# Optimization experiments

Measured on AMD Instinct MI355X. Metric: run time of the kernel, lower is better.

## Reference

```python
import jax, jax.numpy as jnp
import numpy as np

N = 100000   # nodes
E = 1600000  # edges
IN, HID, OUT = 128, 128, 64


def setup_inputs() -> dict:
    key = jax.random.key(0)
    ks = jax.random.split(key, 8)
    x = jax.random.normal(ks[0], (N, IN), dtype=jnp.float32)
    edge_index = jax.random.randint(ks[1], (2, E), 0, N, dtype=jnp.int64)
    W1 = jax.random.normal(ks[2], (IN, HID), dtype=jnp.float32) * 0.05
    b1 = jnp.zeros((HID,), dtype=jnp.float32)
    W2 = jax.random.normal(ks[3], (HID, OUT), dtype=jnp.float32) * 0.05
    b2 = jnp.zeros((OUT,), dtype=jnp.float32)
    Wd = jax.random.normal(ks[4], (OUT, IN), dtype=jnp.float32) * 0.05
    bd = jnp.zeros((IN,), dtype=jnp.float32)
    return {"x": x, "edge_index": edge_index, "W1": W1, "b1": b1,
            "W2": W2, "b2": b2, "Wd": Wd, "bd": bd}


def _gcn_conv(x, src, dst, W, b):
    # PyG GCNConv: add self-loops, symmetric normalization D^-1/2 (A+I) D^-1/2,
    # messages flow src -> dst, aggregated by sum at dst.
    h = x @ W                                   # [N, F]
    ones = jnp.ones((src.shape[0],), x.dtype)
    deg = jax.ops.segment_sum(ones, dst, num_segments=N) + 1.0  # +1 for self-loop
    dinv = jax.lax.rsqrt(deg)                   # deg^-1/2, [N]
    coef = dinv[src] * dinv[dst]                # per-edge norm
    agg = jax.ops.segment_sum(h[src] * coef[:, None], dst, num_segments=N)
    agg = agg + h * (dinv * dinv)[:, None]      # self-loop contribution
    return agg + b


def reference(x, edge_index, W1, b1, W2, b2, Wd, bd):
    src, dst = edge_index[0], edge_index[1]
    h = jax.nn.relu(_gcn_conv(x, src, dst, W1, b1))
    # dropout in eval mode -> identity
    z = _gcn_conv(h, src, dst, W2, b2)          # [N, OUT] embedding
    x_recon = z @ Wd + bd                        # [N, IN]
    return (x_recon, z)
```

## Files before the change

### kernel.cpp

```cpp
#include <hip/hip_runtime.h>
#include <hip/hip_bf16.h>
#include <hip/hip_fp16.h>


#define TPB 256
#define CAP 64

typedef float v2f __attribute__((ext_vector_type(2)));


__device__ __forceinline__ unsigned short f2bf(float f) {
    unsigned u = __float_as_uint(f);
    unsigned r = u + 0x7fffu + ((u >> 16) & 1u);
    return (unsigned short)(r >> 16);
}
__device__ __forceinline__ float bf_lo(unsigned u) { return __uint_as_float(u << 16); }
__device__ __forceinline__ float bf_hi(unsigned u) { return __uint_as_float(u & 0xffff0000u); }


template <int K, int C, int TN, bool BIAS, bool INBF, bool OUTBF>
__device__ __forceinline__ void gemm_body(const void* __restrict__ Ap,
                                          const float* __restrict__ W,
                                          const float* __restrict__ bias,
                                          void* __restrict__ outp, int N, int bid,
                                          float* __restrict__ Ws) {
    constexpr int BM  = 128;
    constexpr int TM  = 8;
    constexpr int BK  = 32;
    constexpr int NCT = C / TN;
    static_assert(NCT * (BM / TM) == TPB, "thread layout");

    int tid = threadIdx.x;
    int tc = tid % NCT;
    int tr = tid / NCT;
    int c0 = tc * TN;
    int r0 = bid * BM + tr * TM;

    float acc[TM][TN] = {};

    for (int k0 = 0; k0 < K; k0 += BK) {
        __syncthreads();
        for (int i = tid * 4; i < BK * C; i += TPB * 4)
            *(float4*)&Ws[i] = *(const float4*)&W[k0 * C + i];
        __syncthreads();

        for (int k = 0; k < BK; k += 4) {
            float4 a[TM];
            uint2  au[TM];
#pragma unroll
            for (int i = 0; i < TM; ++i) {
                int r = r0 + i;
                if (r >= N) r = N - 1;
                if (INBF)
                    au[i] = *(const uint2*)((const unsigned short*)Ap + (size_t)r * K + k0 + k);
                else
                    a[i] = *(const float4*)((const float*)Ap + (size_t)r * K + k0 + k);
            }
#pragma unroll
            for (int kk = 0; kk < 4; ++kk) {
                float w[TN];
#pragma unroll
                for (int j = 0; j < TN; j += 4)
                    *(float4*)&w[j] = *(const float4*)&Ws[(k + kk) * C + c0 + j];
#pragma unroll
                for (int i = 0; i < TM; ++i) {
                    float av;
                    if (INBF) {
                        unsigned uu = (kk < 2) ? au[i].x : au[i].y;
                        av = (kk & 1) ? bf_hi(uu) : bf_lo(uu);
                    } else {
                        av = ((const float*)&a[i])[kk];
                    }
#pragma unroll
                    for (int j = 0; j < TN; ++j) acc[i][j] += av * w[j];
                }
            }
        }
    }

#pragma unroll
    for (int i = 0; i < TM; ++i) {
        int r = r0 + i;
        if (r >= N) continue;
        if (BIAS) {
#pragma unroll
            for (int j = 0; j < TN; ++j) acc[i][j] += bias[c0 + j];
        }
        if (OUTBF) {
            unsigned short* ob = (unsigned short*)outp + (size_t)r * C + c0;
            unsigned pk[TN / 2];
#pragma unroll
            for (int j = 0; j < TN; j += 2)
                pk[j / 2] = (unsigned)f2bf(acc[i][j]) | ((unsigned)f2bf(acc[i][j + 1]) << 16);
            if (TN == 8)      *(uint4*)ob = *(uint4*)pk;
            else if (TN == 4) *(uint2*)ob = *(uint2*)pk;
        } else {
            float* of = (float*)outp + (size_t)r * C + c0;
#pragma unroll
            for (int j = 0; j < TN; j += 4)
                *(float4*)&of[j] = *(float4*)&acc[i][j];
        }
    }
}

template <int K, int C, int TN, bool BIAS, bool INBF, bool OUTBF>
__global__ __launch_bounds__(TPB) void gemm_k(const void* __restrict__ Ap,
                                              const float* __restrict__ W,
                                              const float* __restrict__ bias,
                                              void* __restrict__ outp, int N) {
    __shared__ float Ws[32 * C];
    gemm_body<K, C, TN, BIAS, INBF, OUTBF>(Ap, W, bias, outp, N, blockIdx.x, Ws);
}


__global__ __launch_bounds__(TPB) void fused1_k(const float* __restrict__ x,
                                                const float* __restrict__ W1,
                                                unsigned* __restrict__ h1b,
                                                const int* __restrict__ src,
                                                const int* __restrict__ dst,
                                                int* __restrict__ cnt,
                                                unsigned* __restrict__ bucket,
                                                int N, int E, int gb) {
    __shared__ float Ws[32 * 128];
    if ((int)blockIdx.x < gb) {
        gemm_body<128, 128, 8, false, false, true>(x, W1, nullptr, h1b, N, blockIdx.x, Ws);
    } else {
        int bid = (int)blockIdx.x - gb;
        int e0 = (bid * TPB + (int)threadIdx.x) * 8;
        if (e0 + 7 < E) {
            int4 sa = *(const int4*)&src[e0];
            int4 sb = *(const int4*)&src[e0 + 4];
            int4 da = *(const int4*)&dst[e0];
            int4 db = *(const int4*)&dst[e0 + 4];
            int ss[8] = {sa.x, sa.y, sa.z, sa.w, sb.x, sb.y, sb.z, sb.w};
            int dd[8] = {da.x, da.y, da.z, da.w, db.x, db.y, db.z, db.w};
            int rr[8];
#pragma unroll
            for (int q = 0; q < 8; ++q) rr[q] = atomicAdd(&cnt[dd[q]], 1);
#pragma unroll
            for (int q = 0; q < 8; ++q)
                if (rr[q] < CAP) bucket[(size_t)dd[q] * CAP + rr[q]] = (unsigned)ss[q];
        } else {
            for (int e = e0; e < E; ++e) {
                int s = src[e], d = dst[e];
                int r = atomicAdd(&cnt[d], 1);
                if (r < CAP) bucket[(size_t)d * CAP + r] = (unsigned)s;
            }
        }
    }
}


template <int F2, bool RELU, bool OUTBF>
__global__ __launch_bounds__(TPB) void agg_k(const unsigned* __restrict__ h,
                                             const int* __restrict__ cnt,
                                             const unsigned* __restrict__ bucket,
                                             const float* __restrict__ bias,
                                             void* __restrict__ outp, int N) {
    constexpr int NPB = TPB / F2;
    int ln = threadIdx.x / F2;
    int f2 = threadIdx.x % F2;
    int n  = blockIdx.x * NPB + ln;
    if (n >= N) return;

    int cfull = cnt[n];
    float di = rsqrtf((float)cfull + 1.0f);
    unsigned us = h[(size_t)n * F2 + f2];
    float ax = bf_lo(us) * (di * di);
    float ay = bf_hi(us) * (di * di);

    int cn = cfull < CAP ? cfull : CAP;
    const unsigned* bk = bucket + (size_t)n * CAP;

    int j = 0;
    for (; j + 7 < cn; j += 8) {
        int s[8], cs[8];
        unsigned v[8];
#pragma unroll
        for (int q = 0; q < 8; ++q) s[q] = (int)bk[j + q];
#pragma unroll
        for (int q = 0; q < 8; ++q) {
            v[q]  = h[(size_t)s[q] * F2 + f2];
            cs[q] = cnt[s[q]];
        }
#pragma unroll
        for (int q = 0; q < 8; ++q) {
            float c = rsqrtf((float)cs[q] + 1.0f) * di;
            ax += c * bf_lo(v[q]);
            ay += c * bf_hi(v[q]);
        }
    }
    for (; j < cn; ++j) {
        int s = (int)bk[j];
        unsigned v = h[(size_t)s * F2 + f2];
        float c = rsqrtf((float)cnt[s] + 1.0f) * di;
        ax += c * bf_lo(v);
        ay += c * bf_hi(v);
    }

    float rx = ax + bias[2 * f2];
    float ry = ay + bias[2 * f2 + 1];
    if (RELU) { rx = fmaxf(rx, 0.f); ry = fmaxf(ry, 0.f); }
    if (OUTBF) {
        unsigned pk = (unsigned)f2bf(rx) | ((unsigned)f2bf(ry) << 16);
        ((unsigned*)outp)[(size_t)n * F2 + f2] = pk;
    } else {
        v2f r; r.x = rx; r.y = ry;
        __builtin_nontemporal_store(r, (v2f*)outp + (size_t)n * F2 + f2);
    }
}


extern "C" void kernel_launch(void* const* d_in, const int* in_sizes, int n_in,
                              void* d_out, int out_size, void* d_ws, size_t ws_size,
                              hipStream_t stream) {
    const float* x    = (const float*)d_in[0];
    const int*   eidx = (const int*)d_in[1];
    const float* W1   = (const float*)d_in[2];
    const float* b1   = (const float*)d_in[3];
    const float* W2   = (const float*)d_in[4];
    const float* b2   = (const float*)d_in[5];
    const float* Wd   = (const float*)d_in[6];
    const float* bd   = (const float*)d_in[7];

    const int N = in_sizes[0] / 128;
    const int E = in_sizes[1] / 2;
    const int* src = eidx;
    const int* dst = eidx + E;

    size_t off = 0;
    auto alloc = [&](size_t bytes) {
        void* p = (char*)d_ws + off;
        off += (bytes + 255) & ~(size_t)255;
        return p;
    };
    int*      cnt     = (int*)alloc((size_t)N * 4);
    unsigned* bucket  = (unsigned*)alloc((size_t)N * CAP * 4);
    unsigned* h1b     = (unsigned*)alloc((size_t)N * 64 * 4);
    unsigned* h2b     = (unsigned*)alloc((size_t)N * 32 * 4);
    unsigned* hrelu_b = (unsigned*)alloc((size_t)N * 64 * 4);
    (void)ws_size;

    float* x_recon = (float*)d_out;
    float* z_out   = (float*)d_out + (size_t)N * 128;

    const int gb = (N + 127) / 128;
    const int fb = (E + TPB * 8 - 1) / (TPB * 8);

    (void)hipMemsetAsync(cnt, 0, (size_t)N * 4, stream);

    fused1_k<<<gb + fb, TPB, 0, stream>>>(x, W1, h1b, src, dst, cnt, bucket, N, E, gb);

    agg_k<64, true, true><<<(N + 3) / 4, TPB, 0, stream>>>(h1b, cnt, bucket, b1, hrelu_b, N);
    gemm_k<128, 64, 4, false, true, true><<<gb, TPB, 0, stream>>>(hrelu_b, W2, nullptr, h2b, N);
    agg_k<32, false, false><<<(N + 7) / 8, TPB, 0, stream>>>(h2b, cnt, bucket, b2, z_out, N);
    gemm_k<64, 128, 8, true, false, false><<<gb, TPB, 0, stream>>>(z_out, Wd, bd, x_recon, N);
}
```

Measured before the change: 479.2 us.

## Build edge buckets via two-pass coarse binning with shared-memory scatter

Replaces the per-node global atomic bucket fill with a two-level scheme. Edges are first binned by destination>>6 into coarse bins with packed src/dst-low bits. A second kernel then scatters each bin into per-node buckets in LDS and writes them out coalesced. The GEMM is no longer fused with the edge fill and now runs as a separate launch. This cuts scattered global atomics and writes, but adds an extra pass over the edges and one more launch. The bin capacity of 2048 per 64 nodes and the 26-bit src packing are assumptions that could drop edges on skewed graphs.

```diff
diff --git a/kernel.cpp b/kernel.cpp
--- a/kernel.cpp
+++ b/kernel.cpp
@@ -5,6 +5,8 @@
 
 #define TPB 256
 #define CAP 64
+#define BINSZ 64
+#define BINCAP 2048
 
 typedef float v2f __attribute__((ext_vector_type(2)));
 
@@ -18,23 +20,86 @@
 __device__ __forceinline__ float bf_hi(unsigned u) { return __uint_as_float(u & 0xffff0000u); }
 
 
+__global__ __launch_bounds__(TPB) void binfill_k(const int* __restrict__ src,
+                                                 const int* __restrict__ dst,
+                                                 int* __restrict__ bincnt,
+                                                 unsigned* __restrict__ binbuf, int E) {
+    int e0 = (blockIdx.x * TPB + threadIdx.x) * 8;
+    if (e0 + 7 < E) {
+        int4 sa = *(const int4*)&src[e0];
+        int4 sb = *(const int4*)&src[e0 + 4];
+        int4 da = *(const int4*)&dst[e0];
+        int4 db = *(const int4*)&dst[e0 + 4];
+        int ss[8] = {sa.x, sa.y, sa.z, sa.w, sb.x, sb.y, sb.z, sb.w};
+        int dd[8] = {da.x, da.y, da.z, da.w, db.x, db.y, db.z, db.w};
+        int pp[8];
+#pragma unroll
+        for (int q = 0; q < 8; ++q) pp[q] = atomicAdd(&bincnt[dd[q] >> 6], 1);
+#pragma unroll
+        for (int q = 0; q < 8; ++q) {
+            if (pp[q] < BINCAP)
+                binbuf[(size_t)(dd[q] >> 6) * BINCAP + pp[q]] =
+                    ((unsigned)ss[q] << 6) | (unsigned)(dd[q] & 63);
+        }
+    } else {
+        for (int e = e0; e < E; ++e) {
+            int s = src[e], d = dst[e];
+            int p = atomicAdd(&bincnt[d >> 6], 1);
+            if (p < BINCAP)
+                binbuf[(size_t)(d >> 6) * BINCAP + p] = ((unsigned)s << 6) | (unsigned)(d & 63);
+        }
+    }
+}
+
+
+__global__ __launch_bounds__(TPB) void bucket_k(const int* __restrict__ bincnt,
+                                                const unsigned* __restrict__ binbuf,
+                                                unsigned* __restrict__ bucket,
+                                                int* __restrict__ cnt, int N) {
+    __shared__ unsigned lb[BINSZ * CAP];
+    __shared__ int lc[BINSZ];
+    int b = blockIdx.x;
+    if (threadIdx.x < BINSZ) lc[threadIdx.x] = 0;
+    __syncthreads();
+
+    int m = bincnt[b];
+    if (m > BINCAP) m = BINCAP;
+    const unsigned* bb = binbuf + (size_t)b * BINCAP;
+    for (int i = threadIdx.x; i < m; i += TPB) {
+        unsigned e = bb[i];
+        int d = (int)(e & 63u);
+        int r = atomicAdd(&lc[d], 1);
+        if (r < CAP) lb[d * CAP + r] = e >> 6;
+    }
+    __syncthreads();
+
+    uint4* gout = (uint4*)(bucket + (size_t)b * BINSZ * CAP);
+    const uint4* lin = (const uint4*)lb;
+#pragma unroll 4
+    for (int i = threadIdx.x; i < BINSZ * CAP / 4; i += TPB) gout[i] = lin[i];
+
+    int n0 = b * BINSZ + threadIdx.x;
+    if (threadIdx.x < BINSZ && n0 < N) cnt[n0] = lc[threadIdx.x];
+}
+
+
 template <int K, int C, int TN, bool BIAS, bool INBF, bool OUTBF>
-__device__ __forceinline__ void gemm_body(const void* __restrict__ Ap,
-                                          const float* __restrict__ W,
-                                          const float* __restrict__ bias,
-                                          void* __restrict__ outp, int N, int bid,
-                                          float* __restrict__ Ws) {
+__global__ __launch_bounds__(TPB) void gemm_k(const void* __restrict__ Ap,
+                                              const float* __restrict__ W,
+                                              const float* __restrict__ bias,
+                                              void* __restrict__ outp, int N) {
     constexpr int BM  = 128;
     constexpr int TM  = 8;
     constexpr int BK  = 32;
     constexpr int NCT = C / TN;
     static_assert(NCT * (BM / TM) == TPB, "thread layout");
 
+    __shared__ float Ws[BK * C];
     int tid = threadIdx.x;
     int tc = tid % NCT;
     int tr = tid / NCT;
     int c0 = tc * TN;
-    int r0 = bid * BM + tr * TM;
+    int r0 = blockIdx.x * BM + tr * TM;
 
     float acc[TM][TN] = {};
 
@@ -99,53 +164,6 @@
 #pragma unroll
             for (int j = 0; j < TN; j += 4)
                 *(float4*)&of[j] = *(float4*)&acc[i][j];
-        }
-    }
-}
-
-template <int K, int C, int TN, bool BIAS, bool INBF, bool OUTBF>
-__global__ __launch_bounds__(TPB) void gemm_k(const void* __restrict__ Ap,
-                                              const float* __restrict__ W,
-                                              const float* __restrict__ bias,
-                                              void* __restrict__ outp, int N) {
-    __shared__ float Ws[32 * C];
-    gemm_body<K, C, TN, BIAS, INBF, OUTBF>(Ap, W, bias, outp, N, blockIdx.x, Ws);
-}
-
-
-__global__ __launch_bounds__(TPB) void fused1_k(const float* __restrict__ x,
-                                                const float* __restrict__ W1,
-                                                unsigned* __restrict__ h1b,
-                                                const int* __restrict__ src,
-                                                const int* __restrict__ dst,
-                                                int* __restrict__ cnt,
-                                                unsigned* __restrict__ bucket,
-                                                int N, int E, int gb) {
-    __shared__ float Ws[32 * 128];
-    if ((int)blockIdx.x < gb) {
-        gemm_body<128, 128, 8, false, false, true>(x, W1, nullptr, h1b, N, blockIdx.x, Ws);
-    } else {
-        int bid = (int)blockIdx.x - gb;
-        int e0 = (bid * TPB + (int)threadIdx.x) * 8;
-        if (e0 + 7 < E) {
-            int4 sa = *(const int4*)&src[e0];
-            int4 sb = *(const int4*)&src[e0 + 4];
-            int4 da = *(const int4*)&dst[e0];
-            int4 db = *(const int4*)&dst[e0 + 4];
-            int ss[8] = {sa.x, sa.y, sa.z, sa.w, sb.x, sb.y, sb.z, sb.w};
-            int dd[8] = {da.x, da.y, da.z, da.w, db.x, db.y, db.z, db.w};
-            int rr[8];
-#pragma unroll
-            for (int q = 0; q < 8; ++q) rr[q] = atomicAdd(&cnt[dd[q]], 1);
-#pragma unroll
-            for (int q = 0; q < 8; ++q)
-                if (rr[q] < CAP) bucket[(size_t)dd[q] * CAP + rr[q]] = (unsigned)ss[q];
-        } else {
-            for (int e = e0; e < E; ++e) {
-                int s = src[e], d = dst[e];
-                int r = atomicAdd(&cnt[d], 1);
-                if (r < CAP) bucket[(size_t)d * CAP + r] = (unsigned)s;
-            }
         }
     }
 }
@@ -228,14 +246,18 @@
     const int* src = eidx;
     const int* dst = eidx + E;
 
+    const int K = (N + BINSZ - 1) / BINSZ;
+
     size_t off = 0;
     auto alloc = [&](size_t bytes) {
         void* p = (char*)d_ws + off;
         off += (bytes + 255) & ~(size_t)255;
         return p;
     };
+    int*      bincnt  = (int*)alloc((size_t)K * 4);
+    unsigned* binbuf  = (unsigned*)alloc((size_t)K * BINCAP * 4);
     int*      cnt     = (int*)alloc((size_t)N * 4);
-    unsigned* bucket  = (unsigned*)alloc((size_t)N * CAP * 4);
+    unsigned* bucket  = (unsigned*)alloc((size_t)K * BINSZ * CAP * 4);
     unsigned* h1b     = (unsigned*)alloc((size_t)N * 64 * 4);
     unsigned* h2b     = (unsigned*)alloc((size_t)N * 32 * 4);
     unsigned* hrelu_b = (unsigned*)alloc((size_t)N * 64 * 4);
@@ -245,12 +267,13 @@
     float* z_out   = (float*)d_out + (size_t)N * 128;
 
     const int gb = (N + 127) / 128;
-    const int fb = (E + TPB * 8 - 1) / (TPB * 8);
-
-    (void)hipMemsetAsync(cnt, 0, (size_t)N * 4, stream);
-
-    fused1_k<<<gb + fb, TPB, 0, stream>>>(x, W1, h1b, src, dst, cnt, bucket, N, E, gb);
-
+    const int ab = (E + TPB * 8 - 1) / (TPB * 8);
+
+    (void)hipMemsetAsync(bincnt, 0, (size_t)K * 4, stream);
+    binfill_k<<<ab, TPB, 0, stream>>>(src, dst, bincnt, binbuf, E);
+    bucket_k<<<K, TPB, 0, stream>>>(bincnt, binbuf, bucket, cnt, N);
+
+    gemm_k<128, 128, 8, false, false, true><<<gb, TPB, 0, stream>>>(x, W1, nullptr, h1b, N);
     agg_k<64, true, true><<<(N + 3) / 4, TPB, 0, stream>>>(h1b, cnt, bucket, b1, hrelu_b, N);
     gemm_k<128, 64, 4, false, true, true><<<gb, TPB, 0, stream>>>(hrelu_b, W2, nullptr, h2b, N);
     agg_k<32, false, false><<<(N + 7) / 8, TPB, 0, stream>>>(h2b, cnt, bucket, b2, z_out, N);
```

After: 654.8 us. 1.37x slower.
